# Kernel tuning notes

Hardware: AMD Instinct MI355X
Metric: run time of the kernel (lower is better)

Reference implementation:

```python
import jax, jax.numpy as jnp
import numpy as np

N, E, C, H = 65536, 1048576, 64, 64  # nodes, edges, channels, MLP hidden


def setup_inputs() -> dict:
    key = jax.random.key(0)
    ks = jax.random.split(key, 20)
    w = lambda i, shape: jax.random.normal(ks[i], shape, dtype=jnp.float32) * 0.05
    return {
        "x": jax.random.normal(ks[0], (N, C), dtype=jnp.float32),
        "pos": jax.random.normal(ks[1], (N, 3), dtype=jnp.float32),
        "edge_index": jax.random.randint(ks[2], (2, E), 0, N, dtype=jnp.int32),
        # lin_in / lin_out (with bias)
        "W_in": w(3, (C, C)), "b_in": jnp.zeros((C,), jnp.float32),
        "W_out": w(4, (C, C)), "b_out": jnp.zeros((C,), jnp.float32),
        # PointTransformerConv internal linears (bias=False in PyG)
        "W_lin": w(5, (C, C)), "W_src": w(6, (C, C)), "W_dst": w(7, (C, C)),
        # pos_nn: MLP([3, 64, C], act=leaky_relu, plain_last=False)
        "P1": w(8, (3, H)), "p1": jnp.zeros((H,), jnp.float32),
        "P2": w(9, (H, C)), "p2": jnp.zeros((C,), jnp.float32),
        # attn_nn: MLP([C, 64, C], act=relu, plain_last=False)
        "A1": w(10, (C, H)), "a1": jnp.zeros((H,), jnp.float32),
        "A2": w(11, (H, C)), "a2": jnp.zeros((C,), jnp.float32),
    }


def reference(x, pos, edge_index, W_in, b_in, W_out, b_out, W_lin, W_src, W_dst,
              P1, p1, P2, p2, A1, a1, A2, a2):
    lrelu, relu = jax.nn.leaky_relu, jax.nn.relu
    h = relu(x @ W_in + b_in)                       # [N,C] lin_in + relu
    v = h @ W_lin                                   # value features
    a_src = h @ W_src                               # alpha_j source term
    a_dst = h @ W_dst                               # alpha_i target term
    j, i = edge_index[0], edge_index[1]             # source -> target (PyG flow)
    # pos_nn(pos_i - pos_j): [E,C]
    delta = lrelu(lrelu((pos[i] - pos[j]) @ P1 + p1) @ P2 + p2)
    # attn_nn(alpha_i - alpha_j + delta)
    alpha = relu(relu((a_dst[i] - a_src[j] + delta) @ A1 + a1) @ A2 + a2)
    # scatter softmax over target index i (per channel)
    m = jax.ops.segment_max(alpha, i, num_segments=N)
    m = jnp.where(jnp.isfinite(m), m, 0.0)          # guard empty segments
    e = jnp.exp(alpha - m[i])
    s = jax.ops.segment_sum(e, i, num_segments=N)
    w = e / (s[i] + 1e-16)
    out = jax.ops.segment_sum(w * (v[j] + delta), i, num_segments=N)  # [N,C]
    return relu(out @ W_out + b_out)
```

## Files before the change

kernel.cpp:

```cpp
#include <hip/hip_runtime.h>
#include <hip/hip_bf16.h>

#define NN 65536
#define NE 1048576
#define EW 4096

typedef __attribute__((ext_vector_type(8))) short short8;
typedef __attribute__((ext_vector_type(8))) unsigned short bf16x8;
typedef __attribute__((ext_vector_type(4))) unsigned short bf16x4;
typedef __attribute__((ext_vector_type(4))) float f32x4;
typedef __attribute__((ext_vector_type(4))) unsigned int u32x4;
typedef __attribute__((ext_vector_type(2))) unsigned int u32x2;
typedef __attribute__((ext_vector_type(4))) int i32x4;

__device__ __forceinline__ float lrelu(float x) { return fmaxf(x, 0.01f * x); }
__device__ __forceinline__ float frelu(float x) { return fmaxf(x, 0.f); }
__device__ __forceinline__ short f2bf(float f) {
    __hip_bfloat16 h = __float2bfloat16(f);
    return *reinterpret_cast<short*>(&h);
}
__device__ __forceinline__ float bf2f(unsigned short s) {
    return __uint_as_float(((unsigned)s) << 16);
}
__device__ __forceinline__ unsigned pk2(float lo, float hi) {
    unsigned r;
    asm("v_cvt_pk_bf16_f32 %0, %1, %2" : "=v"(r) : "v"(lo), "v"(hi));
    return r;
}
__device__ __forceinline__ void st4(unsigned short* p, f32x4 v) {
    u32x2 w; w[0] = pk2(v[0], v[1]); w[1] = pk2(v[2], v[3]);
    *(u32x2*)p = w;
}

__global__ void k_pack(const float* __restrict__ P2, const float* __restrict__ A1,
                       const float* __restrict__ A2, const float* __restrict__ Wout,
                       const float* __restrict__ Win, const float* __restrict__ Wlin,
                       const float* __restrict__ Wdst, const float* __restrict__ Wsrc,
                       short* __restrict__ Apack, int* __restrict__ deg) {
    if (blockIdx.x >= 18) {
        int i = (blockIdx.x - 18) * 1024 + threadIdx.x * 4;
        *(i32x4*)(deg + i) = (i32x4)0;
        return;
    }
    int idx = blockIdx.x * 256 + threadIdx.x;
    if (idx >= 9 * 512) return;
    int l = idx & 63, s = (idx >> 6) & 1, rb = (idx >> 7) & 3, fid = idx >> 9;
    const float* Wt[7] = {P2, A1, A2, Wout, Wout, Win, Wlin};
    bool lo = (fid == 4);
#pragma unroll
    for (int b = 0; b < 8; ++b) {
        int in = 32 * s + 8 * (l >> 4) + b;
        int out = 16 * rb + (l & 15);
        float w;
        if (fid >= 7) {
            const float* Wsel = (fid == 7) ? Wdst : Wsrc;
            float acc = 0.f;
            for (int k = 0; k < 64; ++k) acc += Wsel[in * 64 + k] * A1[k * 64 + out];
            w = acc;
        } else {
            w = Wt[fid][in * 64 + out];
            if (fid == 2) w *= 1.44269504088896f;
        }
        short hi = f2bf(w);
        Apack[idx * 8 + b] = lo ? f2bf(w - bf2f((unsigned short)hi)) : hi;
    }
}

__device__ __forceinline__ short8 mkfrag(u32x4 c, int la4, int lb4, bool hi) {
    u32x4 r;
    unsigned a0 = (unsigned)__builtin_amdgcn_ds_bpermute(la4, (int)c[0]);
    unsigned a1 = (unsigned)__builtin_amdgcn_ds_bpermute(la4, (int)c[1]);
    unsigned b0 = (unsigned)__builtin_amdgcn_ds_bpermute(la4, (int)c[2]);
    unsigned b1 = (unsigned)__builtin_amdgcn_ds_bpermute(la4, (int)c[3]);
    r[0] = hi ? b0 : a0; r[1] = hi ? b1 : a1;
    a0 = (unsigned)__builtin_amdgcn_ds_bpermute(lb4, (int)c[0]);
    a1 = (unsigned)__builtin_amdgcn_ds_bpermute(lb4, (int)c[1]);
    b0 = (unsigned)__builtin_amdgcn_ds_bpermute(lb4, (int)c[2]);
    b1 = (unsigned)__builtin_amdgcn_ds_bpermute(lb4, (int)c[3]);
    r[2] = hi ? b0 : a0; r[3] = hi ? b1 : a1;
    return __builtin_bit_cast(short8, r);
}

#define MFMA(a, b, c) __builtin_amdgcn_mfma_f32_16x16x32_bf16(a, b, c, 0, 0, 0)

__global__ void __launch_bounds__(256) k_front(
    const float* __restrict__ x, const float* __restrict__ pos,
    const short* __restrict__ Apack,
    const float* __restrict__ bin, const float* __restrict__ a1,
    const float* __restrict__ P1, const float* __restrict__ p1,
    const int* __restrict__ ei, int* __restrict__ deg, int* __restrict__ eslot,
    int* __restrict__ srtj,
    unsigned short* __restrict__ gsv, unsigned short* __restrict__ nad) {
    if (blockIdx.x >= 4608) {
        int i = (blockIdx.x - 4608) * 1024 + threadIdx.x * 4;
        *(i32x4*)(srtj + i) = (i32x4)0;
        return;
    }
    if (blockIdx.x >= 512) {
        int e = (blockIdx.x - 512) * 256 + threadIdx.x;
        eslot[e] = atomicAdd(&deg[ei[NE + e]], 1);
        return;
    }
    __shared__ short AW2[4 * 4096];
    __shared__ float cb[384];
    {
        const int* gA = (const int*)(Apack + 5 * 4096);
        int* sA = (int*)AW2;
        for (int i = threadIdx.x; i < 8192; i += 256) sA[i] = gA[i];
        if (threadIdx.x < 64) {
            cb[threadIdx.x] = bin[threadIdx.x];
            cb[64 + threadIdx.x] = a1[threadIdx.x];
            cb[128 + threadIdx.x] = p1[threadIdx.x];
        }
        if (threadIdx.x < 192) cb[192 + threadIdx.x] = P1[threadIdx.x];
    }
    __syncthreads();
    int l = threadIdx.x & 63, g = l >> 4, e = l & 15;
    int la4 = (32 * (g & 1) + e) * 4, lb4 = la4 + 64;
    bool hi = (g >= 2);
#define AF2(f, rb, s) (*(const short8*)(AW2 + ((((f) * 4 + (rb)) * 2 + (s)) * 64 + l) * 8))
    int wv = blockIdx.x * 4 + (threadIdx.x >> 6);
    for (int tile = wv; tile < 4096; tile += 2048) {
        int n = tile * 16 + e;
        float p0 = pos[n * 3 + 0], p1v = pos[n * 3 + 1], p2v = pos[n * 3 + 2];
        const float* xr = x + (size_t)n * 64 + 8 * g;
        f32x4 x00 = *(const f32x4*)(xr), x01 = *(const f32x4*)(xr + 4);
        f32x4 x10 = *(const f32x4*)(xr + 32), x11 = *(const f32x4*)(xr + 36);
        short8 xh[2], xl[2];
#pragma unroll
        for (int b = 0; b < 4; ++b) {
            float f;
            f = x00[b]; xh[0][b] = f2bf(f);     xl[0][b] = f2bf(f - bf2f((unsigned short)xh[0][b]));
            f = x01[b]; xh[0][b + 4] = f2bf(f); xl[0][b + 4] = f2bf(f - bf2f((unsigned short)xh[0][b + 4]));
            f = x10[b]; xh[1][b] = f2bf(f);     xl[1][b] = f2bf(f - bf2f((unsigned short)xh[1][b]));
            f = x11[b]; xh[1][b + 4] = f2bf(f); xl[1][b + 4] = f2bf(f - bf2f((unsigned short)xh[1][b + 4]));
        }
        f32x4 acc[4];
#pragma unroll
        for (int rb = 0; rb < 4; ++rb) acc[rb] = *(const f32x4*)(cb + 16 * rb + 4 * g);
#pragma unroll
        for (int rb = 0; rb < 4; ++rb) {
            acc[rb] = MFMA(AF2(0, rb, 0), xh[0], acc[rb]);
            acc[rb] = MFMA(AF2(0, rb, 1), xh[1], acc[rb]);
            acc[rb] = MFMA(AF2(0, rb, 0), xl[0], acc[rb]);
            acc[rb] = MFMA(AF2(0, rb, 1), xl[1], acc[rb]);
        }
        f32x4 hv[4], res[4];
#pragma unroll
        for (int rb = 0; rb < 4; ++rb)
#pragma unroll
            for (int c = 0; c < 4; ++c) {
                float f = frelu(acc[rb][c]);
                hv[rb][c] = f;
                res[rb][c] = f - bf2f((unsigned short)f2bf(f));
            }
        u32x4 HhA, HhB, HlA, HlB;
        HhA[0] = pk2(hv[0][0], hv[0][1]); HhA[1] = pk2(hv[0][2], hv[0][3]);
        HhA[2] = pk2(hv[1][0], hv[1][1]); HhA[3] = pk2(hv[1][2], hv[1][3]);
        HhB[0] = pk2(hv[2][0], hv[2][1]); HhB[1] = pk2(hv[2][2], hv[2][3]);
        HhB[2] = pk2(hv[3][0], hv[3][1]); HhB[3] = pk2(hv[3][2], hv[3][3]);
        HlA[0] = pk2(res[0][0], res[0][1]); HlA[1] = pk2(res[0][2], res[0][3]);
        HlA[2] = pk2(res[1][0], res[1][1]); HlA[3] = pk2(res[1][2], res[1][3]);
        HlB[0] = pk2(res[2][0], res[2][1]); HlB[1] = pk2(res[2][2], res[2][3]);
        HlB[2] = pk2(res[3][0], res[3][1]); HlB[3] = pk2(res[3][2], res[3][3]);
        short8 bhh0 = mkfrag(HhA, la4, lb4, hi), bhh1 = mkfrag(HhB, la4, lb4, hi);
        short8 bhl0 = mkfrag(HlA, la4, lb4, hi), bhl1 = mkfrag(HlB, la4, lb4, hi);

        unsigned short* gr = gsv + (size_t)n * 192;
        unsigned short* nr = nad + (size_t)n * 128;
        f32x4 vres[4];
#pragma unroll
        for (int rb = 0; rb < 4; ++rb) {
            f32x4 a = (f32x4)0.f;
            a = MFMA(AF2(1, rb, 0), bhh0, a);
            a = MFMA(AF2(1, rb, 1), bhh1, a);
            a = MFMA(AF2(1, rb, 0), bhl0, a);
            a = MFMA(AF2(1, rb, 1), bhl1, a);
            vres[rb] = a;
        }
#pragma unroll
        for (int rb = 0; rb < 4; ++rb) {
            f32x4 a = (f32x4)0.f;
            a = MFMA(AF2(3, rb, 0), bhh0, a);
            a = MFMA(AF2(3, rb, 1), bhh1, a);
            a = MFMA(AF2(3, rb, 0), bhl0, a);
            a = MFMA(AF2(3, rb, 1), bhl1, a);
            u32x4 wv4;
            wv4[0] = pk2(a[0], a[1]); wv4[1] = pk2(a[2], a[3]);
            wv4[2] = pk2(vres[rb][0], vres[rb][1]); wv4[3] = pk2(vres[rb][2], vres[rb][3]);
            *(u32x4*)(gr + 64 + 32 * rb + 8 * g) = wv4;
        }
#pragma unroll
        for (int rb = 0; rb < 4; ++rb) {
            f32x4 a = *(const f32x4*)(cb + 64 + 16 * rb + 4 * g);
            a = MFMA(AF2(2, rb, 0), bhh0, a);
            a = MFMA(AF2(2, rb, 1), bhh1, a);
            a = MFMA(AF2(2, rb, 0), bhl0, a);
            a = MFMA(AF2(2, rb, 1), bhl1, a);
            st4(nr + 64 + 16 * rb + 4 * g, a);
        }
#pragma unroll
        for (int rb = 0; rb < 4; ++rb) {
            f32x4 qv, qpv;
#pragma unroll
            for (int c = 0; c < 4; ++c) {
                int ch = 16 * rb + 4 * g + c;
                float q = p0 * cb[192 + ch] + p1v * cb[256 + ch] + p2v * cb[320 + ch];
                qv[c] = q; qpv[c] = q + cb[128 + ch];
            }
            st4(gr + 16 * rb + 4 * g, qv);
            st4(nr + 16 * rb + 4 * g, qpv);
        }
    }
#undef AF2
}

__global__ void __launch_bounds__(1024) k_scan(const int* __restrict__ deg,
                                               int* __restrict__ poff,
                                               int* __restrict__ wstart) {
    __shared__ int part[1024];
    int t = threadIdx.x;
    int base = t * 64;
    int s = 0;
#pragma unroll
    for (int r = 0; r < 64; r += 4) {
        i32x4 d = *(const i32x4*)(deg + base + r);
        s += ((d[0] + 15) & ~15) + ((d[1] + 15) & ~15)
           + ((d[2] + 15) & ~15) + ((d[3] + 15) & ~15);
    }
    part[t] = s;
    __syncthreads();
    int v = s;
    for (int off = 1; off < 1024; off <<= 1) {
        int add = (t >= off) ? part[t - off] : 0;
        __syncthreads();
        v += add; part[t] = v;
        __syncthreads();
    }
    int run = v - s;
#pragma unroll
    for (int r = 0; r < 64; r += 4) {
        i32x4 d = *(const i32x4*)(deg + base + r);
        i32x4 po;
#pragma unroll
        for (int k = 0; k < 4; ++k) { po[k] = run; run += (d[k] + 15) & ~15; }
        *(i32x4*)(poff + base + r) = po;
    }
    if (t == 1023) poff[NN] = run;
    __syncthreads();
    int tot = poff[NN];
    for (int w = t; w < EW; w += 1024) {
        int tgt = (int)(((long long)w * tot) / EW);
        int lo = 0, hi2 = NN;
        while (lo < hi2) { int mid = (lo + hi2) >> 1; if (poff[mid] < tgt) lo = mid + 1; else hi2 = mid; }
        wstart[w] = lo;
    }
    if (t == 0) wstart[EW] = NN;
}

__global__ void k_scatter(const int* __restrict__ ei, const int* __restrict__ eslot,
                          const int* __restrict__ poff, int* __restrict__ srtj) {
    int e = blockIdx.x * 256 + threadIdx.x;
    int i = ei[NE + e];
    srtj[poff[i] + eslot[e]] = ei[e] * 192;
}

__global__ void __launch_bounds__(256) k_edge(
    const unsigned short* __restrict__ gsv, const unsigned short* __restrict__ nad,
    const int* __restrict__ poff, const int* __restrict__ deg,
    const int* __restrict__ srtj, const int* __restrict__ wstart,
    const short* __restrict__ Apack,
    const float* __restrict__ p2b, const float* __restrict__ a2b,
    float* __restrict__ o) {
    __shared__ short AwLds[12288];
    __shared__ float biasLds[128];
    __shared__ unsigned stg[4][768];
    {
        const int* gA = (const int*)Apack;
        int* sA = (int*)AwLds;
        for (int i = threadIdx.x; i < 6144; i += 256) sA[i] = gA[i];
        if (threadIdx.x < 64) {
            biasLds[threadIdx.x] = p2b[threadIdx.x];
            biasLds[64 + threadIdx.x] = a2b[threadIdx.x] * 1.44269504088896f;
        }
    }
    __syncthreads();

    int l = threadIdx.x & 63;
    int g = l >> 4, e = l & 15;
    int w = blockIdx.x * 4 + (threadIdx.x >> 6);

    unsigned* sbw = stg[threadIdx.x >> 6];
    int wbase = (l & 16) ? 2 : 0;
    int tdst1 = 16 * ((l >= 32) ? 1 : 0) + e;
    unsigned* wp0 = sbw + tdst1 * 12 + wbase;
    unsigned* wp1 = wp0 + 4;
    unsigned* wp2 = sbw + (tdst1 + 32) * 12 + wbase;
    unsigned* wp3 = wp2 + 4;
    const unsigned* rp0 = sbw + l * 12;
    const unsigned* rp1 = rp0 + 4;

#define AW(L, rb, s) (*(const short8*)(AwLds + ((((L) * 4 + (rb)) * 2 + (s)) * 64 + l) * 8))
#define XPOSE(cA, cB, f0, f1)                                              \
    {                                                                      \
        u32x2 _a; _a[0] = cA[0]; _a[1] = cA[1]; *(u32x2*)wp0 = _a;         \
        _a[0] = cB[0]; _a[1] = cB[1]; *(u32x2*)wp1 = _a;                   \
        _a[0] = cA[2]; _a[1] = cA[3]; *(u32x2*)wp2 = _a;                   \
        _a[0] = cB[2]; _a[1] = cB[3]; *(u32x2*)wp3 = _a;                   \
        f0 = __builtin_bit_cast(short8, *(const u32x4*)rp0);               \
        f1 = __builtin_bit_cast(short8, *(const u32x4*)rp1);               \
    }

    int node = wstart[w], nodeEnd = wstart[w + 1];
    while (node < nodeEnd && poff[node + 1] == poff[node]) {
        if (e == 0) {
            float* op = o + (size_t)node * 64;
#pragma unroll
            for (int rb = 0; rb < 4; ++rb) *(f32x4*)(op + 16 * rb + 4 * g) = (f32x4)0.f;
        }
        ++node;
    }
    if (node >= nodeEnd) return;

    int t0 = poff[node], t1 = poff[node + 1];
    int vend = t0 + deg[node];
    int tendW = poff[nodeEnd];

    const unsigned short* nr = nad + (size_t)node * 128;
    bf16x8 qpA = *(const bf16x8*)(nr + 8 * g);
    bf16x8 qpB = *(const bf16x8*)(nr + 32 + 8 * g);
    f32x4 advf[4];
#pragma unroll
    for (int rb = 0; rb < 4; ++rb) {
        bf16x4 a = *(const bf16x4*)(nr + 64 + 16 * rb + 4 * g);
#pragma unroll
        for (int c = 0; c < 4; ++c) advf[rb][c] = bf2f(a[c]);
    }

    int prefN = (node + 1 < NN) ? node + 1 : NN - 1;
    const unsigned short* pr = nad + (size_t)prefN * 128;
    bf16x8 pqpA = *(const bf16x8*)(pr + 8 * g);
    bf16x8 pqpB = *(const bf16x8*)(pr + 32 + 8 * g);
    bf16x4 padv[4];
#pragma unroll
    for (int rb = 0; rb < 4; ++rb)
        padv[rb] = *(const bf16x4*)(pr + 64 + 16 * rb + 4 * g);
    int pt1 = poff[prefN + 1];
    int pdeg = deg[prefN];

    f32x4 num[4], den[4];
#pragma unroll
    for (int rb = 0; rb < 4; ++rb) { num[rb] = (f32x4)0.f; den[rb] = (f32x4)0.f; }

    int j1 = srtj[t0 + 16 + e];
    const unsigned short* g0 = gsv + srtj[t0 + e];
    bf16x8 q0A = *(const bf16x8*)(g0 + 8 * g);
    bf16x8 q0B = *(const bf16x8*)(g0 + 32 + 8 * g);
    bf16x8 svld[4];
#pragma unroll
    for (int rb = 0; rb < 4; ++rb)
        svld[rb] = *(const bf16x8*)(g0 + 64 + 32 * rb + 8 * g);

    for (int tb = t0; tb < tendW; tb += 16) {
        int j2 = srtj[tb + 32 + e];
        const unsigned short* g1 = gsv + j1;
        bf16x8 nqA = *(const bf16x8*)(g1 + 8 * g);
        bf16x8 nqB = *(const bf16x8*)(g1 + 32 + 8 * g);

        u32x4 buA, buB;
#pragma unroll
        for (int p = 0; p < 4; ++p) {
            float u0 = lrelu(bf2f(qpA[2 * p]) - bf2f(q0A[2 * p]));
            float u1 = lrelu(bf2f(qpA[2 * p + 1]) - bf2f(q0A[2 * p + 1]));
            buA[p] = pk2(u0, u1);
            u0 = lrelu(bf2f(qpB[2 * p]) - bf2f(q0B[2 * p]));
            u1 = lrelu(bf2f(qpB[2 * p + 1]) - bf2f(q0B[2 * p + 1]));
            buB[p] = pk2(u0, u1);
        }
        short8 bu0 = __builtin_bit_cast(short8, buA);
        short8 bu1 = __builtin_bit_cast(short8, buB);

        f32x4 acc[4];
#pragma unroll
        for (int rb = 0; rb < 4; ++rb) acc[rb] = *(const f32x4*)(biasLds + 16 * rb + 4 * g);
#pragma unroll
        for (int rb = 0; rb < 4; ++rb) {
            acc[rb] = MFMA(AW(0, rb, 0), bu0, acc[rb]);
            acc[rb] = MFMA(AW(0, rb, 1), bu1, acc[rb]);
        }
        f32x4 d4[4];
#pragma unroll
        for (int rb = 0; rb < 4; ++rb)
#pragma unroll
            for (int c = 0; c < 4; ++c) d4[rb][c] = lrelu(acc[rb][c]);
        u32x4 dA, dB;
        dA[0] = pk2(d4[0][0], d4[0][1]); dA[1] = pk2(d4[0][2], d4[0][3]);
        dA[2] = pk2(d4[1][0], d4[1][1]); dA[3] = pk2(d4[1][2], d4[1][3]);
        dB[0] = pk2(d4[2][0], d4[2][1]); dB[1] = pk2(d4[2][2], d4[2][3]);
        dB[2] = pk2(d4[3][0], d4[3][1]); dB[3] = pk2(d4[3][2], d4[3][3]);
        short8 bd0, bd1;
        XPOSE(dA, dB, bd0, bd1);

#pragma unroll
        for (int rb = 0; rb < 4; ++rb) {
            f32x4 t;
#pragma unroll
            for (int c = 0; c < 4; ++c) t[c] = advf[rb][c] - bf2f(svld[rb][c]);
            acc[rb] = t;
        }
#pragma unroll
        for (int rb = 0; rb < 4; ++rb) {
            acc[rb] = MFMA(AW(1, rb, 0), bd0, acc[rb]);
            acc[rb] = MFMA(AW(1, rb, 1), bd1, acc[rb]);
        }
        u32x4 tA, tB;
        tA[0] = pk2(frelu(acc[0][0]), frelu(acc[0][1]));
        tA[1] = pk2(frelu(acc[0][2]), frelu(acc[0][3]));
        tA[2] = pk2(frelu(acc[1][0]), frelu(acc[1][1]));
        tA[3] = pk2(frelu(acc[1][2]), frelu(acc[1][3]));
        tB[0] = pk2(frelu(acc[2][0]), frelu(acc[2][1]));
        tB[1] = pk2(frelu(acc[2][2]), frelu(acc[2][3]));
        tB[2] = pk2(frelu(acc[3][0]), frelu(acc[3][1]));
        tB[3] = pk2(frelu(acc[3][2]), frelu(acc[3][3]));
        short8 bt0, bt1;
        XPOSE(tA, tB, bt0, bt1);

#pragma unroll
        for (int rb = 0; rb < 4; ++rb) acc[rb] = *(const f32x4*)(biasLds + 64 + 16 * rb + 4 * g);
#pragma unroll
        for (int rb = 0; rb < 4; ++rb) {
            acc[rb] = MFMA(AW(2, rb, 0), bt0, acc[rb]);
            acc[rb] = MFMA(AW(2, rb, 1), bt1, acc[rb]);
        }

        bool ok = (tb + e) < vend;
#pragma unroll
        for (int rb = 0; rb < 4; ++rb) {
#pragma unroll
            for (int c = 0; c < 4; ++c) {
                float a = frelu(acc[rb][c]);
                float ew = ok ? exp2f(a) : 0.f;
                den[rb][c] += ew;
                num[rb][c] += ew * (bf2f(svld[rb][4 + c]) + d4[rb][c]);
            }
        }
#pragma unroll
        for (int rb = 0; rb < 4; ++rb)
            svld[rb] = *(const bf16x8*)(g1 + 64 + 32 * rb + 8 * g);

        q0A = nqA; q0B = nqB; j1 = j2;

        if (tb + 16 >= t1) {
#pragma unroll
            for (int m = 1; m < 16; m <<= 1) {
#pragma unroll
                for (int rb = 0; rb < 4; ++rb)
#pragma unroll
                    for (int c = 0; c < 4; ++c) {
                        num[rb][c] += __shfl_xor(num[rb][c], m);
                        den[rb][c] += __shfl_xor(den[rb][c], m);
                    }
            }
            if (e == 0) {
                float* op = o + (size_t)node * 64;
#pragma unroll
                for (int rb = 0; rb < 4; ++rb) {
                    f32x4 ov;
#pragma unroll
                    for (int c = 0; c < 4; ++c)
                        ov[c] = num[rb][c] * __builtin_amdgcn_rcpf(den[rb][c] + 1e-16f);
                    *(f32x4*)(op + 16 * rb + 4 * g) = ov;
                }
            }
            ++node;
            if (node < nodeEnd && node == prefN && pt1 != t1) {
                t0 = t1; t1 = pt1; vend = t0 + pdeg;
                qpA = pqpA; qpB = pqpB;
#pragma unroll
                for (int rb = 0; rb < 4; ++rb)
#pragma unroll
                    for (int c = 0; c < 4; ++c) advf[rb][c] = bf2f(padv[rb][c]);
            } else {
                while (node < nodeEnd && poff[node + 1] == t1) {
                    if (e == 0) {
                        float* op = o + (size_t)node * 64;
#pragma unroll
                        for (int rb = 0; rb < 4; ++rb) *(f32x4*)(op + 16 * rb + 4 * g) = (f32x4)0.f;
                    }
                    ++node;
                }
                if (node < nodeEnd) {
                    t0 = t1; t1 = poff[node + 1];
                    vend = t0 + deg[node];
                    const unsigned short* nr2 = nad + (size_t)node * 128;
                    qpA = *(const bf16x8*)(nr2 + 8 * g);
                    qpB = *(const bf16x8*)(nr2 + 32 + 8 * g);
#pragma unroll
                    for (int rb = 0; rb < 4; ++rb) {
                        bf16x4 a = *(const bf16x4*)(nr2 + 64 + 16 * rb + 4 * g);
#pragma unroll
                        for (int c = 0; c < 4; ++c) advf[rb][c] = bf2f(a[c]);
                    }
                }
            }
            if (node < nodeEnd) {
                prefN = (node + 1 < NN) ? node + 1 : NN - 1;
                const unsigned short* pr2 = nad + (size_t)prefN * 128;
                pqpA = *(const bf16x8*)(pr2 + 8 * g);
                pqpB = *(const bf16x8*)(pr2 + 32 + 8 * g);
#pragma unroll
                for (int rb = 0; rb < 4; ++rb)
                    padv[rb] = *(const bf16x4*)(pr2 + 64 + 16 * rb + 4 * g);
                pt1 = poff[prefN + 1];
                pdeg = deg[prefN];
#pragma unroll
                for (int rb = 0; rb < 4; ++rb) { num[rb] = (f32x4)0.f; den[rb] = (f32x4)0.f; }
            }
        }
    }
#undef AW
#undef XPOSE
}

__global__ void __launch_bounds__(512) k_out(const float* __restrict__ o,
                                             const short* __restrict__ Apack,
                                             const float* __restrict__ bout,
                                             float* __restrict__ out) {
    __shared__ short Ah[4096], Al[4096];
    __shared__ float bb[64];
    {
        const int* gh = (const int*)(Apack + 3 * 4096);
        const int* gl = (const int*)(Apack + 4 * 4096);
        int* sh = (int*)Ah; int* sl = (int*)Al;
        for (int i = threadIdx.x; i < 2048; i += 512) { sh[i] = gh[i]; sl[i] = gl[i]; }
        if (threadIdx.x < 64) bb[threadIdx.x] = bout[threadIdx.x];
    }
    __syncthreads();
    int l = threadIdx.x & 63, g = l >> 4;
    int tile = blockIdx.x * 8 + (threadIdx.x >> 6);
    int nbase = tile * 16;
    const float* op = o + (size_t)(nbase + (l & 15)) * 64;
    f32x4 s0a = *(const f32x4*)(op + 8 * g);
    f32x4 s0b = *(const f32x4*)(op + 8 * g + 4);
    f32x4 s1a = *(const f32x4*)(op + 32 + 8 * g);
    f32x4 s1b = *(const f32x4*)(op + 36 + 8 * g);
    short8 bh0, bl0, bh1, bl1;
#pragma unroll
    for (int b = 0; b < 4; ++b) {
        short h;
        h = f2bf(s0a[b]); bh0[b] = h;     bl0[b] = f2bf(s0a[b] - bf2f((unsigned short)h));
        h = f2bf(s0b[b]); bh0[b + 4] = h; bl0[b + 4] = f2bf(s0b[b] - bf2f((unsigned short)h));
        h = f2bf(s1a[b]); bh1[b] = h;     bl1[b] = f2bf(s1a[b] - bf2f((unsigned short)h));
        h = f2bf(s1b[b]); bh1[b + 4] = h; bl1[b + 4] = f2bf(s1b[b] - bf2f((unsigned short)h));
    }
#define AF(arr, rb, s) (*(const short8*)(arr + (((rb) * 2 + (s)) * 64 + l) * 8))
    f32x4 acc[4];
#pragma unroll
    for (int rb = 0; rb < 4; ++rb) acc[rb] = *(const f32x4*)(bb + 16 * rb + 4 * g);
#pragma unroll
    for (int rb = 0; rb < 4; ++rb) {
        acc[rb] = MFMA(AF(Ah, rb, 0), bh0, acc[rb]);
        acc[rb] = MFMA(AF(Ah, rb, 1), bh1, acc[rb]);
        acc[rb] = MFMA(AF(Ah, rb, 0), bl0, acc[rb]);
        acc[rb] = MFMA(AF(Ah, rb, 1), bl1, acc[rb]);
        acc[rb] = MFMA(AF(Al, rb, 0), bh0, acc[rb]);
        acc[rb] = MFMA(AF(Al, rb, 1), bh1, acc[rb]);
    }
#undef AF
    float* outp = out + (size_t)(nbase + (l & 15)) * 64;
#pragma unroll
    for (int rb = 0; rb < 4; ++rb) {
        f32x4 r;
#pragma unroll
        for (int c = 0; c < 4; ++c) r[c] = frelu(acc[rb][c]);
        *(f32x4*)(outp + 16 * rb + 4 * g) = r;
    }
}

extern "C" void kernel_launch(void* const* d_in, const int* in_sizes, int n_in,
                              void* d_out, int out_size, void* d_ws, size_t ws_size,
                              hipStream_t stream) {
    const float* x    = (const float*)d_in[0];
    const float* pos  = (const float*)d_in[1];
    const int*   ei   = (const int*)d_in[2];
    const float* Win  = (const float*)d_in[3];
    const float* bin  = (const float*)d_in[4];
    const float* Wout = (const float*)d_in[5];
    const float* bout = (const float*)d_in[6];
    const float* Wlin = (const float*)d_in[7];
    const float* Wsrc = (const float*)d_in[8];
    const float* Wdst = (const float*)d_in[9];
    const float* P1   = (const float*)d_in[10];
    const float* p1   = (const float*)d_in[11];
    const float* P2   = (const float*)d_in[12];
    const float* p2   = (const float*)d_in[13];
    const float* A1   = (const float*)d_in[14];
    const float* a1   = (const float*)d_in[15];
    const float* A2   = (const float*)d_in[16];
    const float* a2   = (const float*)d_in[17];
    float* out = (float*)d_out;

    char* w = (char*)d_ws;
    short* Apck = (short*)w; w += 9 * 4096 * 2;
    float* o    = (float*)w; w += (size_t)NN * 64 * 4;
    unsigned short* gsv = (unsigned short*)w; w += (size_t)NN * 192 * 2;
    unsigned short* nad = (unsigned short*)w; w += (size_t)NN * 128 * 2;
    int* deg    = (int*)w; w += (size_t)NN * 4;
    int* poffp  = (int*)w; w += (size_t)(NN + 16) * 4;
    int* eslot  = (int*)w; w += (size_t)NE * 4;
    int* wst    = (int*)w; w += (size_t)(EW + 16) * 4;
    int* srtj   = (int*)w; w += (size_t)2 * NE * 4;

    k_pack<<<18 + 64, 256, 0, stream>>>(P2, A1, A2, Wout, Win, Wlin, Wdst, Wsrc,
                                        Apck, deg);
    k_front<<<512 + 4096 + 2048, 256, 0, stream>>>(x, pos, Apck, bin, a1, P1, p1,
                                                   ei, deg, eslot, srtj, gsv, nad);
    k_scan<<<1, 1024, 0, stream>>>(deg, poffp, wst);
    k_scatter<<<NE / 256, 256, 0, stream>>>(ei, eslot, poffp, srtj);
    k_edge<<<EW / 4, 256, 0, stream>>>(gsv, nad, poffp, deg, srtj, wst, Apck,
                                       p2, a2, o);
    k_out<<<512, 512, 0, stream>>>(o, Apck, bout, out);
}
```

Baseline: 330.1 us.

## Move work-split binary search into edge kernel, one tile per wave in front kernel

Each edge-kernel wave now finds its own start and end node by binary search over the prefix offsets, instead of the single-block scan kernel computing the wstart table. This takes serial work off the one-block scan and lets the search overlap with loading weights into LDS. The front kernel now launches twice as many node-tile blocks with one tile per wave instead of looping over two. It also raises wave priority around the MFMA section of the edge loop. The cost is two extra binary searches per wave in the edge kernel and more blocks in the front kernel.

After: 314.4 us. 1.05x faster.

```diff
diff --git a/kernel.cpp b/kernel.cpp
--- a/kernel.cpp
+++ b/kernel.cpp
@@ -91,13 +91,13 @@
     const int* __restrict__ ei, int* __restrict__ deg, int* __restrict__ eslot,
     int* __restrict__ srtj,
     unsigned short* __restrict__ gsv, unsigned short* __restrict__ nad) {
-    if (blockIdx.x >= 4608) {
-        int i = (blockIdx.x - 4608) * 1024 + threadIdx.x * 4;
+    if (blockIdx.x >= 5120) {
+        int i = (blockIdx.x - 5120) * 1024 + threadIdx.x * 4;
         *(i32x4*)(srtj + i) = (i32x4)0;
         return;
     }
-    if (blockIdx.x >= 512) {
-        int e = (blockIdx.x - 512) * 256 + threadIdx.x;
+    if (blockIdx.x >= 1024) {
+        int e = (blockIdx.x - 1024) * 256 + threadIdx.x;
         eslot[e] = atomicAdd(&deg[ei[NE + e]], 1);
         return;
     }
@@ -119,8 +119,8 @@
     int la4 = (32 * (g & 1) + e) * 4, lb4 = la4 + 64;
     bool hi = (g >= 2);
 #define AF2(f, rb, s) (*(const short8*)(AW2 + ((((f) * 4 + (rb)) * 2 + (s)) * 64 + l) * 8))
-    int wv = blockIdx.x * 4 + (threadIdx.x >> 6);
-    for (int tile = wv; tile < 4096; tile += 2048) {
+    {
+        int tile = blockIdx.x * 4 + (threadIdx.x >> 6);
         int n = tile * 16 + e;
         float p0 = pos[n * 3 + 0], p1v = pos[n * 3 + 1], p2v = pos[n * 3 + 2];
         const float* xr = x + (size_t)n * 64 + 8 * g;
@@ -216,8 +216,7 @@
 }
 
 __global__ void __launch_bounds__(1024) k_scan(const int* __restrict__ deg,
-                                               int* __restrict__ poff,
-                                               int* __restrict__ wstart) {
+                                               int* __restrict__ poff) {
     __shared__ int part[1024];
     int t = threadIdx.x;
     int base = t * 64;
@@ -247,15 +246,6 @@
         *(i32x4*)(poff + base + r) = po;
     }
     if (t == 1023) poff[NN] = run;
-    __syncthreads();
-    int tot = poff[NN];
-    for (int w = t; w < EW; w += 1024) {
-        int tgt = (int)(((long long)w * tot) / EW);
-        int lo = 0, hi2 = NN;
-        while (lo < hi2) { int mid = (lo + hi2) >> 1; if (poff[mid] < tgt) lo = mid + 1; else hi2 = mid; }
-        wstart[w] = lo;
-    }
-    if (t == 0) wstart[EW] = NN;
 }
 
 __global__ void k_scatter(const int* __restrict__ ei, const int* __restrict__ eslot,
@@ -268,8 +258,7 @@
 __global__ void __launch_bounds__(256) k_edge(
     const unsigned short* __restrict__ gsv, const unsigned short* __restrict__ nad,
     const int* __restrict__ poff, const int* __restrict__ deg,
-    const int* __restrict__ srtj, const int* __restrict__ wstart,
-    const short* __restrict__ Apack,
+    const int* __restrict__ srtj, const short* __restrict__ Apack,
     const float* __restrict__ p2b, const float* __restrict__ a2b,
     float* __restrict__ o) {
     __shared__ short AwLds[12288];
@@ -284,11 +273,28 @@
             biasLds[64 + threadIdx.x] = a2b[threadIdx.x] * 1.44269504088896f;
         }
     }
-    __syncthreads();
 
     int l = threadIdx.x & 63;
     int g = l >> 4, e = l & 15;
     int w = blockIdx.x * 4 + (threadIdx.x >> 6);
+
+    int tot = poff[NN];
+    int node, nodeEnd;
+    {
+        long long t1l = (long long)w * tot;
+        int tgt = (int)(t1l / EW);
+        int lo = 0, hi2 = NN;
+        while (lo < hi2) { int mid = (lo + hi2) >> 1; if (poff[mid] < tgt) lo = mid + 1; else hi2 = mid; }
+        node = lo;
+        if (w + 1 == EW) nodeEnd = NN;
+        else {
+            int tgt2 = (int)((t1l + tot) / EW);
+            lo = 0; hi2 = NN;
+            while (lo < hi2) { int mid = (lo + hi2) >> 1; if (poff[mid] < tgt2) lo = mid + 1; else hi2 = mid; }
+            nodeEnd = lo;
+        }
+    }
+    __syncthreads();
 
     unsigned* sbw = stg[threadIdx.x >> 6];
     int wbase = (l & 16) ? 2 : 0;
@@ -311,7 +317,6 @@
         f1 = __builtin_bit_cast(short8, *(const u32x4*)rp1);               \
     }
 
-    int node = wstart[w], nodeEnd = wstart[w + 1];
     while (node < nodeEnd && poff[node + 1] == poff[node]) {
         if (e == 0) {
             float* op = o + (size_t)node * 64;
@@ -380,6 +385,7 @@
         short8 bu0 = __builtin_bit_cast(short8, buA);
         short8 bu1 = __builtin_bit_cast(short8, buB);
 
+        __builtin_amdgcn_s_setprio(1);
         f32x4 acc[4];
 #pragma unroll
         for (int rb = 0; rb < 4; ++rb) acc[rb] = *(const f32x4*)(biasLds + 16 * rb + 4 * g);
@@ -432,6 +438,7 @@
             acc[rb] = MFMA(AW(2, rb, 0), bt0, acc[rb]);
             acc[rb] = MFMA(AW(2, rb, 1), bt1, acc[rb]);
         }
+        __builtin_amdgcn_s_setprio(0);
 
         bool ok = (tb + e) < vend;
 #pragma unroll
@@ -608,16 +615,15 @@
     int* deg    = (int*)w; w += (size_t)NN * 4;
     int* poffp  = (int*)w; w += (size_t)(NN + 16) * 4;
     int* eslot  = (int*)w; w += (size_t)NE * 4;
-    int* wst    = (int*)w; w += (size_t)(EW + 16) * 4;
     int* srtj   = (int*)w; w += (size_t)2 * NE * 4;
 
     k_pack<<<18 + 64, 256, 0, stream>>>(P2, A1, A2, Wout, Win, Wlin, Wdst, Wsrc,
                                         Apck, deg);
-    k_front<<<512 + 4096 + 2048, 256, 0, stream>>>(x, pos, Apck, bin, a1, P1, p1,
-                                                   ei, deg, eslot, srtj, gsv, nad);
-    k_scan<<<1, 1024, 0, stream>>>(deg, poffp, wst);
+    k_front<<<1024 + 4096 + 2048, 256, 0, stream>>>(x, pos, Apck, bin, a1, P1, p1,
+                                                    ei, deg, eslot, srtj, gsv, nad);
+    k_scan<<<1, 1024, 0, stream>>>(deg, poffp);
     k_scatter<<<NE / 256, 256, 0, stream>>>(ei, eslot, poffp, srtj);
-    k_edge<<<EW / 4, 256, 0, stream>>>(gsv, nad, poffp, deg, srtj, wst, Apck,
+    k_edge<<<EW / 4, 256, 0, stream>>>(gsv, nad, poffp, deg, srtj, Apck,
                                        p2, a2, o);
     k_out<<<512, 512, 0, stream>>>(o, Apck, bout, out);
 }
```
